# Kernel tuning notes

Measured on AMD Instinct MI355X. Metric: run time of the kernel, lower is better.

The kernel has to match this reference:

```python
import jax, jax.numpy as jnp
import numpy as np

K = 3  # kernel_size

def setup_inputs() -> dict:
    key = jax.random.key(0)
    k1, k2, k3 = jax.random.split(key, 3)
    B, C, H, W = 8, 64, 128, 128
    x = jax.random.normal(k1, (B, C, H, W), dtype=jnp.float32)
    # 1x1 conv weight (out_channels*K*K, in_channels) and bias
    W_gen = jax.random.normal(k2, (C * K * K, C), dtype=jnp.float32) / np.float32(np.sqrt(C))
    b_gen = jax.random.normal(k3, (C * K * K,), dtype=jnp.float32) * 0.01
    return {"x": x, "W_gen": W_gen, "b_gen": b_gen}

def reference(x, W_gen, b_gen):
    B, C, H, W = x.shape  # out_channels == in_channels (required by the view)
    # filter_gen: 1x1 conv + ReLU -> (B, C*K*K, H, W)
    f = jax.nn.relu(jnp.einsum('bchw,oc->bohw', x, W_gen) + b_gen[None, :, None, None])
    filters = f.reshape(B, C, K * K, H, W)
    # F.unfold with padding=(K-1)//2, stride 1: gather KxK patches per pixel.
    pad = (K - 1) // 2
    xp = jnp.pad(x, ((0, 0), (0, 0), (pad, pad), (pad, pad)))
    # kernel-position index runs row-major (i*K + j), matching unfold layout
    patches = jnp.stack([xp[:, :, i:i + H, j:j + W]
                         for i in range(K) for j in range(K)], axis=2)  # (B,C,K*K,H,W)
    out = (filters * patches).sum(axis=2)  # (B,C,H,W)
    return out
```

## Files before the change

### kernel.cpp

```cpp
#include <hip/hip_runtime.h>
#include <hip/hip_bf16.h>

#define CC 64
#define HH 128
#define WW 128
#define OO 576
#define HW (HH * WW)

typedef __attribute__((ext_vector_type(8))) short short8;
typedef __attribute__((ext_vector_type(4))) short short4v;
typedef __attribute__((ext_vector_type(4))) float floatx4;

__device__ __forceinline__ unsigned short f2bf(float f) {
    unsigned u = __float_as_uint(f);
    u = (u + 0x7FFFu + ((u >> 16) & 1u)) >> 16;
    return (unsigned short)u;
}

__device__ __forceinline__ float bf2f(short s) {
    return __uint_as_float(((unsigned)(unsigned short)s) << 16);
}

__device__ __forceinline__ short8 pack8(floatx4 a, floatx4 b) {
    __hip_bfloat162 p0 = __float22bfloat162_rn(make_float2(a[0], a[1]));
    __hip_bfloat162 p1 = __float22bfloat162_rn(make_float2(a[2], a[3]));
    __hip_bfloat162 p2 = __float22bfloat162_rn(make_float2(b[0], b[1]));
    __hip_bfloat162 p3 = __float22bfloat162_rn(make_float2(b[2], b[3]));
    unsigned u0, u1, u2, u3;
    __builtin_memcpy(&u0, &p0, 4); __builtin_memcpy(&u1, &p1, 4);
    __builtin_memcpy(&u2, &p2, 4); __builtin_memcpy(&u3, &p3, 4);
    short8 v;
    v[0] = (short)(u0 & 0xffffu); v[1] = (short)(u0 >> 16);
    v[2] = (short)(u1 & 0xffffu); v[3] = (short)(u1 >> 16);
    v[4] = (short)(u2 & 0xffffu); v[5] = (short)(u2 >> 16);
    v[6] = (short)(u3 & 0xffffu); v[7] = (short)(u3 >> 16);
    return v;
}

__global__ void ACDA_wconv_kernel(const float* __restrict__ Wg,
                                  const float* __restrict__ bg,
                                  unsigned short* __restrict__ Wb,
                                  float* __restrict__ Bp) {
    int i = blockIdx.x * 256 + threadIdx.x;
    if (i < OO * CC) {
        int o2  = i >> 6;
        int col = i & 63;
        int kk  = o2 >> 6;
        int c   = o2 & 63;
        Wb[i] = f2bf(Wg[(c * 9 + kk) * CC + col]);
    }
    if (i < OO) Bp[i] = bg[(i & 63) * 9 + (i >> 6)];
}

__global__ __launch_bounds__(256, 5) void ACDA_main_kernel(
    const float* __restrict__ x, const unsigned short* __restrict__ Wb,
    const float* __restrict__ Bp, float* __restrict__ out)
{
    __shared__ short S[3][66][72];

    const int tid  = threadIdx.x;
    const int lane = tid & 63;
    const int wv   = tid >> 6;
    const int quad = lane >> 4;
    const int l16  = lane & 15;
    const int c0   = wv * 16;

    const int bid = blockIdx.x;
    const int wk  = (bid & 7) * 256 + (bid >> 3);
    const int seg = wk & 1;
    const int h   = (wk >> 1) & 127;
    const int b   = wk >> 8;
    const int w0  = seg << 6;

    const float* xb = x + (size_t)b * CC * HW;

#pragma unroll
    for (int di = 0; di < 3; ++di) {
        const int hh = h + di - 1;
        const bool oob = (hh < 0) || (hh > 127);
        const int hc = hh < 0 ? 0 : (hh > 127 ? 127 : hh);
        const float* src = xb + hc * WW + w0 + lane;
#pragma unroll
        for (int hf = 0; hf < 2; ++hf) {
            const int c = c0 + 8 * hf;
            short8 v8;
            if (!oob) {
                floatx4 va, vb;
                va[0] = src[(c + 0) * HW]; va[1] = src[(c + 1) * HW];
                va[2] = src[(c + 2) * HW]; va[3] = src[(c + 3) * HW];
                vb[0] = src[(c + 4) * HW]; vb[1] = src[(c + 5) * HW];
                vb[2] = src[(c + 6) * HW]; vb[3] = src[(c + 7) * HW];
                v8 = pack8(va, vb);
            } else {
                v8 = short8{0, 0, 0, 0, 0, 0, 0, 0};
            }
            *(short8*)&S[di][lane + 1][c] = v8;
        }
    }
    if (tid < 192) {
        const int di = tid >> 6, c = tid & 63;
        const int hh = h + di - 1;
        const bool oob = (hh < 0) || (hh > 127);
        const int hc = hh < 0 ? 0 : (hh > 127 ? 127 : hh);
        unsigned short vL = 0, vR = 0;
        if (!oob) {
            if (w0 > 0)       vL = f2bf(xb[c * HW + hc * WW + w0 - 1]);
            if (w0 + 64 < WW) vR = f2bf(xb[c * HW + hc * WW + w0 + 64]);
        }
        S[di][0][c]  = (short)vL;
        S[di][65][c] = (short)vR;
    }
    __syncthreads();

    short8 bfrag[4][2];
#pragma unroll
    for (int nt = 0; nt < 4; ++nt)
#pragma unroll
        for (int ks = 0; ks < 2; ++ks)
            bfrag[nt][ks] = *(const short8*)&S[1][nt * 16 + l16 + 1][ks * 32 + quad * 8];

    floatx4 acc[4];
#pragma unroll
    for (int nt = 0; nt < 4; ++nt) acc[nt] = floatx4{0.f, 0.f, 0.f, 0.f};

#pragma unroll
    for (int t = 0; t < 9; ++t) {
        const int di = t / 3;
        const int dj = t - 3 * di;
        const unsigned short* wrow = Wb + (t * 64 + c0 + l16) * CC + quad * 8;
        short8 a0 = *(const short8*)(wrow);
        short8 a1 = *(const short8*)(wrow + 32);
        floatx4 bv = *(const floatx4*)(Bp + t * 64 + c0 + 4 * quad);
#pragma unroll
        for (int nt = 0; nt < 4; ++nt) {
            short4v ph = *(const short4v*)&S[di][nt * 16 + l16 + dj][c0 + 4 * quad];
            floatx4 z = bv;
            z = __builtin_amdgcn_mfma_f32_16x16x32_bf16(a0, bfrag[nt][0], z, 0, 0, 0);
            z = __builtin_amdgcn_mfma_f32_16x16x32_bf16(a1, bfrag[nt][1], z, 0, 0, 0);
#pragma unroll
            for (int rg = 0; rg < 4; ++rg)
                acc[nt][rg] = fmaf(fmaxf(z[rg], 0.f), bf2f(ph[rg]), acc[nt][rg]);
        }
    }

    float* ob = out + (size_t)b * CC * HW + h * WW + w0;
#pragma unroll
    for (int nt = 0; nt < 4; ++nt)
#pragma unroll
        for (int rg = 0; rg < 4; ++rg)
            ob[(c0 + 4 * quad + rg) * HW + nt * 16 + l16] = acc[nt][rg];
}

extern "C" void kernel_launch(void* const* d_in, const int* in_sizes, int n_in,
                              void* d_out, int out_size, void* d_ws, size_t ws_size,
                              hipStream_t stream) {
    const float* x  = (const float*)d_in[0];
    const float* Wg = (const float*)d_in[1];
    const float* bg = (const float*)d_in[2];
    float* out = (float*)d_out;
    unsigned short* Wb = (unsigned short*)d_ws;
    float* Bp = (float*)((char*)d_ws + OO * CC * 2);

    ACDA_wconv_kernel<<<dim3((OO * CC + 255) / 256), dim3(256), 0, stream>>>(Wg, bg, Wb, Bp);
    ACDA_main_kernel<<<dim3(8 * 128 * 2), dim3(256), 0, stream>>>(x, Wb, Bp, out);
}
```

Before: 110.6 us.

## Process two output rows per block to share halo rows in LDS

Each block now covers two adjacent output rows with 512 threads (8 waves), staging four input rows in LDS instead of three per single row. This cuts redundant global loads of the halo rows from 3x to 2x per output row and halves the block count. In exchange, LDS per block grows and launch bounds change to 512 threads with a min-blocks hint of 8, which may raise register pressure.

```diff
diff --git a/kernel.cpp b/kernel.cpp
--- a/kernel.cpp
+++ b/kernel.cpp
@@ -52,63 +52,62 @@
     if (i < OO) Bp[i] = bg[(i & 63) * 9 + (i >> 6)];
 }
 
-__global__ __launch_bounds__(256, 5) void ACDA_main_kernel(
+__global__ __launch_bounds__(512, 8) void ACDA_main_kernel(
     const float* __restrict__ x, const unsigned short* __restrict__ Wb,
     const float* __restrict__ Bp, float* __restrict__ out)
 {
-    __shared__ short S[3][66][72];
+    __shared__ short S[4][66][72];
 
     const int tid  = threadIdx.x;
     const int lane = tid & 63;
-    const int wv   = tid >> 6;
+    const int g    = tid >> 6;
+    const int hw   = g & 1;
+    const int cg   = g >> 1;
     const int quad = lane >> 4;
     const int l16  = lane & 15;
-    const int c0   = wv * 16;
+    const int c0   = cg * 16;
 
     const int bid = blockIdx.x;
-    const int wk  = (bid & 7) * 256 + (bid >> 3);
+    const int wk  = (bid & 7) * 128 + (bid >> 3);
     const int seg = wk & 1;
-    const int h   = (wk >> 1) & 127;
-    const int b   = wk >> 8;
+    const int hp  = (wk >> 1) & 63;
+    const int b   = wk >> 7;
     const int w0  = seg << 6;
+    const int h0  = hp << 1;
 
     const float* xb = x + (size_t)b * CC * HW;
 
 #pragma unroll
-    for (int di = 0; di < 3; ++di) {
-        const int hh = h + di - 1;
+    for (int r = 0; r < 4; ++r) {
+        const int hh = h0 + r - 1;
         const bool oob = (hh < 0) || (hh > 127);
         const int hc = hh < 0 ? 0 : (hh > 127 ? 127 : hh);
         const float* src = xb + hc * WW + w0 + lane;
-#pragma unroll
-        for (int hf = 0; hf < 2; ++hf) {
-            const int c = c0 + 8 * hf;
-            short8 v8;
-            if (!oob) {
-                floatx4 va, vb;
-                va[0] = src[(c + 0) * HW]; va[1] = src[(c + 1) * HW];
-                va[2] = src[(c + 2) * HW]; va[3] = src[(c + 3) * HW];
-                vb[0] = src[(c + 4) * HW]; vb[1] = src[(c + 5) * HW];
-                vb[2] = src[(c + 6) * HW]; vb[3] = src[(c + 7) * HW];
-                v8 = pack8(va, vb);
-            } else {
-                v8 = short8{0, 0, 0, 0, 0, 0, 0, 0};
-            }
-            *(short8*)&S[di][lane + 1][c] = v8;
+        const int c = g * 8;
+        short8 v8 = short8{0, 0, 0, 0, 0, 0, 0, 0};
+        if (!oob) {
+            floatx4 va, vb;
+            va[0] = src[(c + 0) * HW]; va[1] = src[(c + 1) * HW];
+            va[2] = src[(c + 2) * HW]; va[3] = src[(c + 3) * HW];
+            vb[0] = src[(c + 4) * HW]; vb[1] = src[(c + 5) * HW];
+            vb[2] = src[(c + 6) * HW]; vb[3] = src[(c + 7) * HW];
+            v8 = pack8(va, vb);
         }
+        *(short8*)&S[r][lane + 1][c] = v8;
     }
-    if (tid < 192) {
-        const int di = tid >> 6, c = tid & 63;
-        const int hh = h + di - 1;
+    {
+        const int r4   = tid >> 7;
+        const int idx  = tid & 127;
+        const int c    = idx >> 1;
+        const int side = idx & 1;
+        const int hh = h0 + r4 - 1;
         const bool oob = (hh < 0) || (hh > 127);
         const int hc = hh < 0 ? 0 : (hh > 127 ? 127 : hh);
-        unsigned short vL = 0, vR = 0;
-        if (!oob) {
-            if (w0 > 0)       vL = f2bf(xb[c * HW + hc * WW + w0 - 1]);
-            if (w0 + 64 < WW) vR = f2bf(xb[c * HW + hc * WW + w0 + 64]);
-        }
-        S[di][0][c]  = (short)vL;
-        S[di][65][c] = (short)vR;
+        const int col = side ? (w0 + 64) : (w0 - 1);
+        unsigned short v = 0;
+        if (!oob && col >= 0 && col < WW)
+            v = f2bf(xb[c * HW + hc * WW + col]);
+        S[r4][side ? 65 : 0][c] = (short)v;
     }
     __syncthreads();
 
@@ -117,7 +116,7 @@
     for (int nt = 0; nt < 4; ++nt)
 #pragma unroll
         for (int ks = 0; ks < 2; ++ks)
-            bfrag[nt][ks] = *(const short8*)&S[1][nt * 16 + l16 + 1][ks * 32 + quad * 8];
+            bfrag[nt][ks] = *(const short8*)&S[hw + 1][nt * 16 + l16 + 1][ks * 32 + quad * 8];
 
     floatx4 acc[4];
 #pragma unroll
@@ -133,7 +132,7 @@
         floatx4 bv = *(const floatx4*)(Bp + t * 64 + c0 + 4 * quad);
 #pragma unroll
         for (int nt = 0; nt < 4; ++nt) {
-            short4v ph = *(const short4v*)&S[di][nt * 16 + l16 + dj][c0 + 4 * quad];
+            short4v ph = *(const short4v*)&S[hw + di][nt * 16 + l16 + dj][c0 + 4 * quad];
             floatx4 z = bv;
             z = __builtin_amdgcn_mfma_f32_16x16x32_bf16(a0, bfrag[nt][0], z, 0, 0, 0);
             z = __builtin_amdgcn_mfma_f32_16x16x32_bf16(a1, bfrag[nt][1], z, 0, 0, 0);
@@ -143,7 +142,7 @@
         }
     }
 
-    float* ob = out + (size_t)b * CC * HW + h * WW + w0;
+    float* ob = out + (size_t)b * CC * HW + (h0 + hw) * WW + w0;
 #pragma unroll
     for (int nt = 0; nt < 4; ++nt)
 #pragma unroll
@@ -162,5 +161,5 @@
     float* Bp = (float*)((char*)d_ws + OO * CC * 2);
 
     ACDA_wconv_kernel<<<dim3((OO * CC + 255) / 256), dim3(256), 0, stream>>>(Wg, bg, Wb, Bp);
-    ACDA_main_kernel<<<dim3(8 * 128 * 2), dim3(256), 0, stream>>>(x, Wb, Bp, out);
+    ACDA_main_kernel<<<dim3(8 * 64 * 2), dim3(512), 0, stream>>>(x, Wb, Bp, out);
 }
```

Result: slower. 197.3 us (+78.5%).
